# Kernel optimization log

Hardware: AMD Instinct MI355X
Metric: run time of the kernel (lower is better)

The kernel has to match this reference:

```python
import jax, jax.numpy as jnp
import numpy as np

B, T, C = 4, 2048, 1024
N_HEAD = 16
HEAD_DIM = C // N_HEAD


def setup_inputs() -> dict:
    key = jax.random.key(0)
    kx, kk, kq, kv, kp = jax.random.split(key, 5)
    s = 1.0 / np.sqrt(C)
    return {
        "x": jax.random.normal(kx, (B, T, C), dtype=jnp.float32),
        "Wk": jax.random.normal(kk, (C, C), dtype=jnp.float32) * s,
        "Wq": jax.random.normal(kq, (C, C), dtype=jnp.float32) * s,
        "Wv": jax.random.normal(kv, (C, C), dtype=jnp.float32) * s,
        "Wp": jax.random.normal(kp, (C, C), dtype=jnp.float32) * s,
    }


def reference(x, Wk, Wq, Wv, Wp):
    b, t, c = x.shape
    # torch nn.Linear(y = x @ W.T); split heads -> [B, H, T, D]
    def heads(w):
        return jnp.einsum("btc,ec->bte", x, w).reshape(b, t, N_HEAD, HEAD_DIM).transpose(0, 2, 1, 3)
    k = heads(Wk)
    q = heads(Wq)
    v = heads(Wv)
    scale = 1.0 / np.sqrt(HEAD_DIM).astype(np.float32)
    att = jnp.einsum("bhqd,bhkd->bhqk", q, k) * scale  # [B,H,T,T]
    causal = jnp.tril(jnp.ones((t, t), dtype=bool))
    att = jnp.where(causal[None, None], att, -jnp.inf)
    att = jax.nn.softmax(att, axis=-1)
    y = jnp.einsum("bhqk,bhkd->bhqd", att, v)  # [B,H,T,D]
    y = y.transpose(0, 2, 1, 3).reshape(b, t, c)
    return jnp.einsum("btc,ec->bte", y, Wp)
```

## Files before the change

### kernel.cpp

```cpp
#include <hip/hip_runtime.h>

typedef __bf16 bf16x8 __attribute__((ext_vector_type(8)));
typedef float f32x4 __attribute__((ext_vector_type(4)));
typedef float f32x16 __attribute__((ext_vector_type(16)));
typedef unsigned short u16x8 __attribute__((ext_vector_type(8)));
typedef unsigned short u16x4 __attribute__((ext_vector_type(4)));
typedef unsigned u32x4 __attribute__((ext_vector_type(4)));

#define BB 4
#define TT 2048
#define CC 1024
#define HH 16
#define DD 64

__device__ __forceinline__ unsigned short f2bf(float f){
  unsigned u = __builtin_bit_cast(unsigned, f);
  u += 0x7FFFu + ((u >> 16) & 1u);
  return (unsigned short)(u >> 16);
}
__device__ __forceinline__ bf16x8 as_bf(u16x8 v){ return __builtin_bit_cast(bf16x8, v); }
__device__ __forceinline__ unsigned cvt_pk(float lo, float hi){
  unsigned r; asm("v_cvt_pk_bf16_f32 %0, %1, %2" : "=v"(r) : "v"(lo), "v"(hi)); return r;
}
__device__ __forceinline__ void pl32swap(unsigned &a, unsigned &b){
  asm("v_permlane32_swap_b32 %0, %1" : "+v"(a), "+v"(b));
}
__device__ __forceinline__ float ex2(float x){
#if __has_builtin(__builtin_amdgcn_exp2f)
  return __builtin_amdgcn_exp2f(x);
#else
  return __expf(x * 0.6931471805599453f);
#endif
}

__global__ __launch_bounds__(256) void cvt_all(const float* __restrict__ x,
                                               const float* __restrict__ Wk,
                                               const float* __restrict__ Wq,
                                               const float* __restrict__ Wv,
                                               const float* __restrict__ Wp,
                                               unsigned short* __restrict__ xb,
                                               unsigned short* __restrict__ wb){
  const int i = blockIdx.x * 256 + threadIdx.x;
  constexpr int EX = (BB*TT*CC)/4;
  const float* src; unsigned short* dst; int off;
  if (i < EX){ src = x; dst = xb; off = i; }
  else {
    const int j = i - EX;
    const int wsel = j >> 18;
    off = j & 262143;
    src = (wsel==0) ? Wk : (wsel==1) ? Wq : (wsel==2) ? Wv : Wp;
    dst = wb + ((size_t)wsel << 20);
  }
  const float4 f = ((const float4*)src)[off];
  u16x4 o; o.x = f2bf(f.x); o.y = f2bf(f.y); o.z = f2bf(f.z); o.w = f2bf(f.w);
  ((u16x4*)dst)[off] = o;
}

template<int NX, bool QKV>
__global__ __launch_bounds__(256) void gemm128(const unsigned short* __restrict__ A,
                                               const unsigned short* __restrict__ Bm,
                                               void* __restrict__ o0, void* __restrict__ o1,
                                               void* __restrict__ o2){
  constexpr int K = 1024;
  constexpr int NWG = NX * 64;
  __shared__ __align__(16) unsigned short As[128*64];
  __shared__ __align__(16) unsigned short Bs[128*64];
  const int tid = threadIdx.x;
  const int flat = blockIdx.y * NX + blockIdx.x;
  const int swz = (flat & 7) * (NWG / 8) + (flat >> 3);
  const int n0 = (swz % NX) * 128;
  const int m0 = (swz / NX) * 128;
  const int w = tid >> 6, lane = tid & 63, l15 = lane & 15, g = lane >> 4;
  const int wm = (w >> 1) * 64, wn = (w & 1) * 64;

  f32x4 acc[4][4] = {};

  for (int k0 = 0; k0 < K; k0 += 64){
    #pragma unroll
    for (int i = 0; i < 4; ++i){
      const int p = i*256 + tid;
      const int r = p >> 3, c = p & 7;
      const int gc = c ^ (r & 7);
      __builtin_amdgcn_global_load_lds(
        (const __attribute__((address_space(1))) void*)(A + (size_t)(m0 + r)*K + k0 + gc*8),
        (__attribute__((address_space(3))) void*)(As + p*8), 16, 0, 0);
    }
    #pragma unroll
    for (int i = 0; i < 4; ++i){
      const int p = i*256 + tid;
      const int r = p >> 3, c = p & 7;
      const int gc = c ^ (r & 7);
      __builtin_amdgcn_global_load_lds(
        (const __attribute__((address_space(1))) void*)(Bm + (size_t)(n0 + r)*K + k0 + gc*8),
        (__attribute__((address_space(3))) void*)(Bs + p*8), 16, 0, 0);
    }
    __syncthreads();

    bf16x8 af[2][4], bfr[2][4];
    #pragma unroll
    for (int ks = 0; ks < 2; ++ks){
      #pragma unroll
      for (int m = 0; m < 4; ++m){
        const int R = wm + m*16 + l15;
        const int c = (ks*4 + g) ^ (R & 7);
        af[ks][m] = as_bf(*(const u16x8*)(As + R*64 + c*8));
      }
      #pragma unroll
      for (int n = 0; n < 4; ++n){
        const int R = wn + n*16 + l15;
        const int c = (ks*4 + g) ^ (R & 7);
        bfr[ks][n] = as_bf(*(const u16x8*)(Bs + R*64 + c*8));
      }
    }
    #pragma unroll
    for (int ks = 0; ks < 2; ++ks)
      #pragma unroll
      for (int m = 0; m < 4; ++m)
        #pragma unroll
        for (int n = 0; n < 4; ++n)
          acc[m][n] = __builtin_amdgcn_mfma_f32_16x16x32_bf16(af[ks][m], bfr[ks][n], acc[m][n], 0, 0, 0);
    __syncthreads();
  }

  const int tsel = n0 >> 10;
  const float sc = (QKV && tsel == 1) ? 0.18033688011112042f : 1.0f;
  unsigned short* outb = nullptr;
  if (QKV) outb = (unsigned short*)(tsel == 0 ? o0 : tsel == 1 ? o1 : o2);

  #pragma unroll
  for (int m = 0; m < 4; ++m)
    #pragma unroll
    for (int n = 0; n < 4; ++n)
      #pragma unroll
      for (int r = 0; r < 4; ++r){
        const int row = m0 + wm + m*16 + g*4 + r;
        const int col = n0 + wn + n*16 + l15;
        const float v = acc[m][n][r];
        if (QKV) outb[(size_t)row*1024 + (col & 1023)] = f2bf(v * sc);
        else     ((float*)o0)[(size_t)row*1024 + col] = v;
      }
}

__global__ __launch_bounds__(256) void transpose_v(const unsigned short* __restrict__ V,
                                                   unsigned short* __restrict__ Vt){
  __shared__ unsigned short Ts[64*72];
  const int kt = blockIdx.x, bh = blockIdx.y;
  const int b = bh >> 4, h = bh & 15;
  const int tid = threadIdx.x;
  #pragma unroll
  for (int i = 0; i < 2; ++i){
    const int p = i*256 + tid, r = p >> 3, c = p & 7;
    *(u16x8*)(Ts + r*72 + c*8) =
      *(const u16x8*)(V + (size_t)b*TT*CC + (size_t)(kt*64 + r)*CC + h*DD + c*8);
  }
  __syncthreads();
  #pragma unroll
  for (int i = 0; i < 2; ++i){
    const int p = i*256 + tid, d = p >> 3, c = p & 7;
    u16x8 v;
    #pragma unroll
    for (int j = 0; j < 8; ++j) v[j] = Ts[(c*8 + j)*72 + d];
    *(u16x8*)(Vt + ((size_t)bh*DD + d)*TT + (size_t)kt*64 + ((c ^ (d & 7))*8)) = v;
  }
}

__global__ __launch_bounds__(512, 4) void attn2(const unsigned short* __restrict__ Q,
                                                const unsigned short* __restrict__ Km,
                                                const unsigned short* __restrict__ Vt,
                                                unsigned short* __restrict__ Y){
  __shared__ __align__(16) unsigned short Ks[3][64*64];
  __shared__ __align__(16) unsigned short Vs[3][64*64];
  const int bh = blockIdx.x, b = bh >> 4, h = bh & 15;
  const int qt = 7 - blockIdx.y;
  const int tid = threadIdx.x;
  const int w = tid >> 6, lane = tid & 63, l31 = lane & 31, hi = lane >> 5;
  const int q0 = qt * 256;
  const int wq0 = q0 + w * 32;
  const int wqmax = wq0 + 31;
  const int nkt = 4 * qt + 4;
  const int qg = wq0 + l31;

  const unsigned short* Ksrc = Km + (size_t)b*TT*CC + h*DD;
  const unsigned short* Vsrc = Vt + (size_t)bh*DD*TT;

  auto stage = [&](int buf, int kt){
    const int r = tid >> 3, c = tid & 7;
    const int gc = c ^ (r & 7);
    __builtin_amdgcn_global_load_lds(
      (const __attribute__((address_space(1))) void*)(Ksrc + (size_t)(kt*64 + r)*CC + gc*8),
      (__attribute__((address_space(3))) void*)(&Ks[buf][tid*8]), 16, 0, 0);
    __builtin_amdgcn_global_load_lds(
      (const __attribute__((address_space(1))) void*)(Vsrc + (size_t)r*TT + (size_t)kt*64 + c*8),
      (__attribute__((address_space(3))) void*)(&Vs[buf][tid*8]), 16, 0, 0);
  };

  stage(0, 0);

  const unsigned short* qrow = Q + ((size_t)b*TT + wq0 + l31)*CC + h*DD;
  bf16x8 qf[4];
  #pragma unroll
  for (int ds = 0; ds < 4; ++ds)
    qf[ds] = as_bf(*(const u16x8*)(qrow + 16*ds + 8*hi));

  int koff[4];
  #pragma unroll
  for (int ds = 0; ds < 4; ++ds)
    koff[ds] = l31*64 + (((2*ds + hi) ^ (l31 & 7)) * 8);

  float m_ = -1e30f, l_ = 0.f;
  f32x16 y0 = {}, y1 = {};

  int cb = 0;
  for (int t = 0; t < nkt; ++t){
    const int nx = (cb == 2) ? 0 : cb + 1;
    if (t + 1 < nkt){
      stage(nx, t + 1);
      asm volatile("s_waitcnt vmcnt(2)" ::: "memory");
    } else {
      asm volatile("s_waitcnt vmcnt(0)" ::: "memory");
    }
    __builtin_amdgcn_s_barrier();

    if (t*64 <= wqmax){
      const unsigned short* Kp = &Ks[cb][0];
      const unsigned short* Vp = &Vs[cb][0];

      f32x16 s0 = {}, s1 = {};
      __builtin_amdgcn_s_setprio(1);
      #pragma unroll
      for (int ds = 0; ds < 4; ++ds){
        bf16x8 kf0 = as_bf(*(const u16x8*)(Kp + koff[ds]));
        s0 = __builtin_amdgcn_mfma_f32_32x32x16_bf16(kf0, qf[ds], s0, 0, 0, 0);
        bf16x8 kf1 = as_bf(*(const u16x8*)(Kp + koff[ds] + 2048));
        s1 = __builtin_amdgcn_mfma_f32_32x32x16_bf16(kf1, qf[ds], s1, 0, 0, 0);
      }
      __builtin_amdgcn_s_setprio(0);

      if (t*64 + 63 > wq0){
        const int kb0 = t*64;
        #pragma unroll
        for (int r = 0; r < 16; ++r){
          const int kr = (r & 3) + 8*(r >> 2) + 4*hi;
          if (kb0 + kr      > qg) s0[r] = -1e30f;
          if (kb0 + 32 + kr > qg) s1[r] = -1e30f;
        }
      }

      float tm[8];
      #pragma unroll
      for (int r = 0; r < 8; ++r) tm[r] = fmaxf(fmaxf(s0[r], s0[r+8]), fmaxf(s1[r], s1[r+8]));
      #pragma unroll
      for (int r = 0; r < 4; ++r) tm[r] = fmaxf(tm[r], tm[r+4]);
      float pmax = fmaxf(fmaxf(tm[0], tm[2]), fmaxf(tm[1], tm[3]));
      pmax = fmaxf(pmax, __shfl_xor(pmax, 32));

      if (!__all(pmax <= m_ + 8.f)){
        const float mnew = fmaxf(m_, pmax);
        const float alpha = ex2(m_ - mnew);
        l_ *= alpha;
        #pragma unroll
        for (int r = 0; r < 16; ++r){
          const float ar = __shfl(alpha, (r & 3) + 8*(r >> 2) + 4*hi);
          y0[r] *= ar; y1[r] *= ar;
        }
        m_ = mnew;
      }

      #pragma unroll
      for (int r = 0; r < 16; ++r) s0[r] = ex2(s0[r] - m_);
      #pragma unroll
      for (int r = 0; r < 16; ++r) s1[r] = ex2(s1[r] - m_);
      float ts[8];
      #pragma unroll
      for (int r = 0; r < 8; ++r) ts[r] = (s0[r] + s0[r+8]) + (s1[r] + s1[r+8]);
      #pragma unroll
      for (int r = 0; r < 4; ++r) ts[r] += ts[r+4];
      float rs = (ts[0] + ts[2]) + (ts[1] + ts[3]);
      rs += __shfl_xor(rs, 32);
      l_ += rs;

      __builtin_amdgcn_s_setprio(1);
      #pragma unroll
      for (int m = 0; m < 4; ++m){
        const f32x16 c = (m < 2) ? s0 : s1;
        const int bx = (m & 1) * 8;
        unsigned A0 = cvt_pk(c[bx+0], c[bx+1]);
        unsigned B0 = cvt_pk(c[bx+4], c[bx+5]);
        pl32swap(A0, B0);
        unsigned A1 = cvt_pk(c[bx+2], c[bx+3]);
        unsigned B1 = cvt_pk(c[bx+6], c[bx+7]);
        pl32swap(A1, B1);
        u32x4 pw; pw.x = A0; pw.y = A1; pw.z = B0; pw.w = B1;
        const bf16x8 pa = __builtin_bit_cast(bf16x8, pw);
        bf16x8 vf0 = as_bf(*(const u16x8*)(Vp + koff[m]));
        y0 = __builtin_amdgcn_mfma_f32_32x32x16_bf16(pa, vf0, y0, 0, 0, 0);
        bf16x8 vf1 = as_bf(*(const u16x8*)(Vp + koff[m] + 2048));
        y1 = __builtin_amdgcn_mfma_f32_32x32x16_bf16(pa, vf1, y1, 0, 0, 0);
      }
      __builtin_amdgcn_s_setprio(0);
    }
    cb = nx;
  }

  const float linv = 1.f / l_;
  #pragma unroll
  for (int r = 0; r < 16; ++r){
    const int qlr = (r & 3) + 8*(r >> 2) + 4*hi;
    const float lr = __shfl(linv, qlr);
    unsigned short* yp = Y + ((size_t)b*TT + wq0 + qlr)*CC + h*DD + l31;
    yp[0]  = f2bf(y0[r] * lr);
    yp[32] = f2bf(y1[r] * lr);
  }
}

extern "C" void kernel_launch(void* const* d_in, const int* in_sizes, int n_in,
                              void* d_out, int out_size, void* d_ws, size_t ws_size,
                              hipStream_t stream){
  const float* x  = (const float*)d_in[0];
  const float* Wk = (const float*)d_in[1];
  const float* Wq = (const float*)d_in[2];
  const float* Wv = (const float*)d_in[3];
  const float* Wp = (const float*)d_in[4];

  const size_t E  = (size_t)BB*TT*CC;
  const size_t Wn = (size_t)CC*CC;
  unsigned short* ws  = (unsigned short*)d_ws;
  unsigned short* xb  = ws;
  unsigned short* wkb = xb  + E;
  unsigned short* wqb = wkb + Wn;
  unsigned short* wvb = wqb + Wn;
  unsigned short* wpb = wvb + Wn;
  unsigned short* qb  = wpb + Wn;
  unsigned short* kb  = qb  + E;
  unsigned short* vb  = kb  + E;
  unsigned short* vt  = vb  + E;

  cvt_all<<<12288, 256, 0, stream>>>(x, Wk, Wq, Wv, Wp, xb, wkb);

  gemm128<24, true><<<dim3(24, 64), 256, 0, stream>>>(xb, wkb, kb, qb, vb);

  transpose_v<<<dim3(TT/64, BB*HH), 256, 0, stream>>>(vb, vt);

  unsigned short* yb = xb;
  attn2<<<dim3(BB*HH, TT/256), 512, 0, stream>>>(qb, kb, vt, yb);

  gemm128<8, false><<<dim3(8, 64), 256, 0, stream>>>(yb, wpb, (float*)d_out, nullptr, nullptr);
}
```

Measured before the change: 164.2 us.

## Give each attention wave two query tiles and deepen K/V prefetch

The attention kernel now runs 256 threads per block, and each wave handles 64 query rows as two 32-row tiles. Each K/V fragment read from LDS therefore feeds two MFMAs, halving LDS reads per unit of math. The K/V staging ring grows from 3 to 4 buffers with a prefetch distance of two tiles to hide global load latency. This raises register pressure (four score and four output accumulators per wave), and with fewer waves per block, causal-skip imbalance across waves could leave some waves idle longer.

```diff
diff --git a/kernel.cpp b/kernel.cpp
--- a/kernel.cpp
+++ b/kernel.cpp
@@ -164,153 +164,179 @@
   }
 }
 
-__global__ __launch_bounds__(512, 4) void attn2(const unsigned short* __restrict__ Q,
+__global__ __launch_bounds__(256, 2) void attn3(const unsigned short* __restrict__ Q,
                                                 const unsigned short* __restrict__ Km,
                                                 const unsigned short* __restrict__ Vt,
                                                 unsigned short* __restrict__ Y){
-  __shared__ __align__(16) unsigned short Ks[3][64*64];
-  __shared__ __align__(16) unsigned short Vs[3][64*64];
-  const int bh = blockIdx.x, b = bh >> 4, h = bh & 15;
+  __shared__ __align__(16) unsigned short Ks[4][64*64];
+  __shared__ __align__(16) unsigned short Vs[4][64*64];
+  const int bh = blockIdx.x, b = bh >> 4, hd = bh & 15;
   const int qt = 7 - blockIdx.y;
   const int tid = threadIdx.x;
   const int w = tid >> 6, lane = tid & 63, l31 = lane & 31, hi = lane >> 5;
-  const int q0 = qt * 256;
-  const int wq0 = q0 + w * 32;
-  const int wqmax = wq0 + 31;
-  const int nkt = 4 * qt + 4;
-  const int qg = wq0 + l31;
-
-  const unsigned short* Ksrc = Km + (size_t)b*TT*CC + h*DD;
+  const int nkt = 4*qt + 4;
+  const int qbase = qt*256 + w*64;
+  const int tD = 4*qt + w;
+  const int qga = qbase + l31, qgb = qbase + 32 + l31;
+
+  const unsigned short* Ksrc = Km + (size_t)b*TT*CC + hd*DD;
   const unsigned short* Vsrc = Vt + (size_t)bh*DD*TT;
 
   auto stage = [&](int buf, int kt){
-    const int r = tid >> 3, c = tid & 7;
-    const int gc = c ^ (r & 7);
-    __builtin_amdgcn_global_load_lds(
-      (const __attribute__((address_space(1))) void*)(Ksrc + (size_t)(kt*64 + r)*CC + gc*8),
-      (__attribute__((address_space(3))) void*)(&Ks[buf][tid*8]), 16, 0, 0);
-    __builtin_amdgcn_global_load_lds(
-      (const __attribute__((address_space(1))) void*)(Vsrc + (size_t)r*TT + (size_t)kt*64 + c*8),
-      (__attribute__((address_space(3))) void*)(&Vs[buf][tid*8]), 16, 0, 0);
+    #pragma unroll
+    for (int i = 0; i < 2; ++i){
+      const int rr = (tid >> 3) + i*32, c = tid & 7;
+      const int gc = c ^ (rr & 7);
+      __builtin_amdgcn_global_load_lds(
+        (const __attribute__((address_space(1))) void*)(Ksrc + (size_t)(kt*64 + rr)*CC + gc*8),
+        (__attribute__((address_space(3))) void*)(&Ks[buf][(i*256 + tid)*8]), 16, 0, 0);
+      __builtin_amdgcn_global_load_lds(
+        (const __attribute__((address_space(1))) void*)(Vsrc + (size_t)rr*TT + (size_t)kt*64 + c*8),
+        (__attribute__((address_space(3))) void*)(&Vs[buf][(i*256 + tid)*8]), 16, 0, 0);
+    }
   };
 
   stage(0, 0);
-
-  const unsigned short* qrow = Q + ((size_t)b*TT + wq0 + l31)*CC + h*DD;
-  bf16x8 qf[4];
-  #pragma unroll
-  for (int ds = 0; ds < 4; ++ds)
-    qf[ds] = as_bf(*(const u16x8*)(qrow + 16*ds + 8*hi));
+  stage(1, 1);
+
+  const unsigned short* qra = Q + ((size_t)b*TT + qbase + l31)*CC + hd*DD;
+  bf16x8 qfA[4], qfB[4];
+  #pragma unroll
+  for (int ds = 0; ds < 4; ++ds){
+    qfA[ds] = as_bf(*(const u16x8*)(qra + 16*ds + 8*hi));
+    qfB[ds] = as_bf(*(const u16x8*)(qra + 32*CC + 16*ds + 8*hi));
+  }
 
   int koff[4];
   #pragma unroll
   for (int ds = 0; ds < 4; ++ds)
     koff[ds] = l31*64 + (((2*ds + hi) ^ (l31 & 7)) * 8);
 
-  float m_ = -1e30f, l_ = 0.f;
-  f32x16 y0 = {}, y1 = {};
-
-  int cb = 0;
+  float mA = -1e30f, lA = 0.f, mB = -1e30f, lB = 0.f;
+  f32x16 yA0 = {}, yA1 = {}, yB0 = {}, yB1 = {};
+
+  auto sm = [&](f32x16& s0, f32x16& s1, float& m_, float& l_, f32x16& y0, f32x16& y1){
+    float tm[8];
+    #pragma unroll
+    for (int r = 0; r < 8; ++r) tm[r] = fmaxf(fmaxf(s0[r], s0[r+8]), fmaxf(s1[r], s1[r+8]));
+    #pragma unroll
+    for (int r = 0; r < 4; ++r) tm[r] = fmaxf(tm[r], tm[r+4]);
+    float pmax = fmaxf(fmaxf(tm[0], tm[2]), fmaxf(tm[1], tm[3]));
+    pmax = fmaxf(pmax, __shfl_xor(pmax, 32));
+    if (!__all(pmax <= m_ + 8.f)){
+      const float mnew = fmaxf(m_, pmax);
+      const float alpha = ex2(m_ - mnew);
+      l_ *= alpha;
+      #pragma unroll
+      for (int r = 0; r < 16; ++r){
+        const float ar = __shfl(alpha, (r & 3) + 8*(r >> 2) + 4*hi);
+        y0[r] *= ar; y1[r] *= ar;
+      }
+      m_ = mnew;
+    }
+    #pragma unroll
+    for (int r = 0; r < 16; ++r) s0[r] = ex2(s0[r] - m_);
+    #pragma unroll
+    for (int r = 0; r < 16; ++r) s1[r] = ex2(s1[r] - m_);
+    float ts[8];
+    #pragma unroll
+    for (int r = 0; r < 8; ++r) ts[r] = (s0[r] + s0[r+8]) + (s1[r] + s1[r+8]);
+    #pragma unroll
+    for (int r = 0; r < 4; ++r) ts[r] += ts[r+4];
+    float rs = (ts[0] + ts[2]) + (ts[1] + ts[3]);
+    rs += __shfl_xor(rs, 32);
+    l_ += rs;
+  };
+
+  auto pack = [&](const f32x16& s0, const f32x16& s1, bf16x8* pa){
+    #pragma unroll
+    for (int m = 0; m < 4; ++m){
+      const f32x16& c = (m < 2) ? s0 : s1;
+      const int bx = (m & 1) * 8;
+      unsigned A0 = cvt_pk(c[bx+0], c[bx+1]);
+      unsigned B0 = cvt_pk(c[bx+4], c[bx+5]);
+      pl32swap(A0, B0);
+      unsigned A1 = cvt_pk(c[bx+2], c[bx+3]);
+      unsigned B1 = cvt_pk(c[bx+6], c[bx+7]);
+      pl32swap(A1, B1);
+      u32x4 pw; pw.x = A0; pw.y = A1; pw.z = B0; pw.w = B1;
+      pa[m] = __builtin_bit_cast(bf16x8, pw);
+    }
+  };
+
   for (int t = 0; t < nkt; ++t){
-    const int nx = (cb == 2) ? 0 : cb + 1;
-    if (t + 1 < nkt){
-      stage(nx, t + 1);
-      asm volatile("s_waitcnt vmcnt(2)" ::: "memory");
+    if (t + 2 < nkt){
+      stage((t + 2) & 3, t + 2);
+      asm volatile("s_waitcnt vmcnt(8)" ::: "memory");
+    } else if (t + 1 < nkt){
+      asm volatile("s_waitcnt vmcnt(4)" ::: "memory");
     } else {
       asm volatile("s_waitcnt vmcnt(0)" ::: "memory");
     }
     __builtin_amdgcn_s_barrier();
-
-    if (t*64 <= wqmax){
-      const unsigned short* Kp = &Ks[cb][0];
-      const unsigned short* Vp = &Vs[cb][0];
-
-      f32x16 s0 = {}, s1 = {};
-      __builtin_amdgcn_s_setprio(1);
-      #pragma unroll
-      for (int ds = 0; ds < 4; ++ds){
-        bf16x8 kf0 = as_bf(*(const u16x8*)(Kp + koff[ds]));
-        s0 = __builtin_amdgcn_mfma_f32_32x32x16_bf16(kf0, qf[ds], s0, 0, 0, 0);
-        bf16x8 kf1 = as_bf(*(const u16x8*)(Kp + koff[ds] + 2048));
-        s1 = __builtin_amdgcn_mfma_f32_32x32x16_bf16(kf1, qf[ds], s1, 0, 0, 0);
-      }
-      __builtin_amdgcn_s_setprio(0);
-
-      if (t*64 + 63 > wq0){
-        const int kb0 = t*64;
-        #pragma unroll
-        for (int r = 0; r < 16; ++r){
-          const int kr = (r & 3) + 8*(r >> 2) + 4*hi;
-          if (kb0 + kr      > qg) s0[r] = -1e30f;
-          if (kb0 + 32 + kr > qg) s1[r] = -1e30f;
-        }
-      }
-
-      float tm[8];
-      #pragma unroll
-      for (int r = 0; r < 8; ++r) tm[r] = fmaxf(fmaxf(s0[r], s0[r+8]), fmaxf(s1[r], s1[r+8]));
-      #pragma unroll
-      for (int r = 0; r < 4; ++r) tm[r] = fmaxf(tm[r], tm[r+4]);
-      float pmax = fmaxf(fmaxf(tm[0], tm[2]), fmaxf(tm[1], tm[3]));
-      pmax = fmaxf(pmax, __shfl_xor(pmax, 32));
-
-      if (!__all(pmax <= m_ + 8.f)){
-        const float mnew = fmaxf(m_, pmax);
-        const float alpha = ex2(m_ - mnew);
-        l_ *= alpha;
-        #pragma unroll
-        for (int r = 0; r < 16; ++r){
-          const float ar = __shfl(alpha, (r & 3) + 8*(r >> 2) + 4*hi);
-          y0[r] *= ar; y1[r] *= ar;
-        }
-        m_ = mnew;
-      }
-
-      #pragma unroll
-      for (int r = 0; r < 16; ++r) s0[r] = ex2(s0[r] - m_);
-      #pragma unroll
-      for (int r = 0; r < 16; ++r) s1[r] = ex2(s1[r] - m_);
-      float ts[8];
-      #pragma unroll
-      for (int r = 0; r < 8; ++r) ts[r] = (s0[r] + s0[r+8]) + (s1[r] + s1[r+8]);
-      #pragma unroll
-      for (int r = 0; r < 4; ++r) ts[r] += ts[r+4];
-      float rs = (ts[0] + ts[2]) + (ts[1] + ts[3]);
-      rs += __shfl_xor(rs, 32);
-      l_ += rs;
-
-      __builtin_amdgcn_s_setprio(1);
-      #pragma unroll
-      for (int m = 0; m < 4; ++m){
-        const f32x16 c = (m < 2) ? s0 : s1;
-        const int bx = (m & 1) * 8;
-        unsigned A0 = cvt_pk(c[bx+0], c[bx+1]);
-        unsigned B0 = cvt_pk(c[bx+4], c[bx+5]);
-        pl32swap(A0, B0);
-        unsigned A1 = cvt_pk(c[bx+2], c[bx+3]);
-        unsigned B1 = cvt_pk(c[bx+6], c[bx+7]);
-        pl32swap(A1, B1);
-        u32x4 pw; pw.x = A0; pw.y = A1; pw.z = B0; pw.w = B1;
-        const bf16x8 pa = __builtin_bit_cast(bf16x8, pw);
-        bf16x8 vf0 = as_bf(*(const u16x8*)(Vp + koff[m]));
-        y0 = __builtin_amdgcn_mfma_f32_32x32x16_bf16(pa, vf0, y0, 0, 0, 0);
-        bf16x8 vf1 = as_bf(*(const u16x8*)(Vp + koff[m] + 2048));
-        y1 = __builtin_amdgcn_mfma_f32_32x32x16_bf16(pa, vf1, y1, 0, 0, 0);
-      }
-      __builtin_amdgcn_s_setprio(0);
-    }
-    cb = nx;
-  }
-
-  const float linv = 1.f / l_;
-  #pragma unroll
-  for (int r = 0; r < 16; ++r){
-    const int qlr = (r & 3) + 8*(r >> 2) + 4*hi;
-    const float lr = __shfl(linv, qlr);
-    unsigned short* yp = Y + ((size_t)b*TT + wq0 + qlr)*CC + h*DD + l31;
-    yp[0]  = f2bf(y0[r] * lr);
-    yp[32] = f2bf(y1[r] * lr);
-  }
+    if (t > tD) continue;
+
+    const unsigned short* Kp = &Ks[t & 3][0];
+    const unsigned short* Vp = &Vs[t & 3][0];
+
+    f32x16 sA0 = {}, sA1 = {}, sB0 = {}, sB1 = {};
+    __builtin_amdgcn_s_setprio(1);
+    #pragma unroll
+    for (int ds = 0; ds < 4; ++ds){
+      bf16x8 kf0 = as_bf(*(const u16x8*)(Kp + koff[ds]));
+      sA0 = __builtin_amdgcn_mfma_f32_32x32x16_bf16(kf0, qfA[ds], sA0, 0, 0, 0);
+      sB0 = __builtin_amdgcn_mfma_f32_32x32x16_bf16(kf0, qfB[ds], sB0, 0, 0, 0);
+      bf16x8 kf1 = as_bf(*(const u16x8*)(Kp + koff[ds] + 2048));
+      sA1 = __builtin_amdgcn_mfma_f32_32x32x16_bf16(kf1, qfA[ds], sA1, 0, 0, 0);
+      sB1 = __builtin_amdgcn_mfma_f32_32x32x16_bf16(kf1, qfB[ds], sB1, 0, 0, 0);
+    }
+    __builtin_amdgcn_s_setprio(0);
+
+    if (t == tD){
+      const int kb0 = t*64;
+      #pragma unroll
+      for (int r = 0; r < 16; ++r){
+        const int kr = (r & 3) + 8*(r >> 2) + 4*hi;
+        if (kb0 + kr      > qga) sA0[r] = -1e30f;
+        if (kb0 + 32 + kr > qga) sA1[r] = -1e30f;
+        if (kb0 + kr      > qgb) sB0[r] = -1e30f;
+        if (kb0 + 32 + kr > qgb) sB1[r] = -1e30f;
+      }
+    }
+
+    sm(sA0, sA1, mA, lA, yA0, yA1);
+    sm(sB0, sB1, mB, lB, yB0, yB1);
+
+    bf16x8 paA[4], paB[4];
+    pack(sA0, sA1, paA);
+    pack(sB0, sB1, paB);
+
+    __builtin_amdgcn_s_setprio(1);
+    #pragma unroll
+    for (int m = 0; m < 4; ++m){
+      bf16x8 vf0 = as_bf(*(const u16x8*)(Vp + koff[m]));
+      yA0 = __builtin_amdgcn_mfma_f32_32x32x16_bf16(paA[m], vf0, yA0, 0, 0, 0);
+      yB0 = __builtin_amdgcn_mfma_f32_32x32x16_bf16(paB[m], vf0, yB0, 0, 0, 0);
+      bf16x8 vf1 = as_bf(*(const u16x8*)(Vp + koff[m] + 2048));
+      yA1 = __builtin_amdgcn_mfma_f32_32x32x16_bf16(paA[m], vf1, yA1, 0, 0, 0);
+      yB1 = __builtin_amdgcn_mfma_f32_32x32x16_bf16(paB[m], vf1, yB1, 0, 0, 0);
+    }
+    __builtin_amdgcn_s_setprio(0);
+  }
+
+  auto wr = [&](const f32x16& y0, const f32x16& y1, float l_, int qb){
+    const float linv = 1.f / l_;
+    #pragma unroll
+    for (int r = 0; r < 16; ++r){
+      const int qlr = (r & 3) + 8*(r >> 2) + 4*hi;
+      const float lr = __shfl(linv, qlr);
+      unsigned short* yp = Y + ((size_t)b*TT + qb + qlr)*CC + hd*DD + l31;
+      yp[0]  = f2bf(y0[r] * lr);
+      yp[32] = f2bf(y1[r] * lr);
+    }
+  };
+  wr(yA0, yA1, lA, qbase);
+  wr(yB0, yB1, lB, qbase + 32);
 }
 
 extern "C" void kernel_launch(void* const* d_in, const int* in_sizes, int n_in,
@@ -342,7 +368,7 @@
   transpose_v<<<dim3(TT/64, BB*HH), 256, 0, stream>>>(vb, vt);
 
   unsigned short* yb = xb;
-  attn2<<<dim3(BB*HH, TT/256), 512, 0, stream>>>(qb, kb, vt, yb);
+  attn3<<<dim3(BB*HH, TT/256), 256, 0, stream>>>(qb, kb, vt, yb);
 
   gemm128<8, false><<<dim3(8, 64), 256, 0, stream>>>(yb, wpb, (float*)d_out, nullptr, nullptr);
 }
```

Result: slower. 177.2 us (+7.9%).

## Double-buffer GEMM LDS tiles and reorder attention query-tile scheduling

Applied to the files above, without the earlier changes.

The 128x128 GEMM kernel now keeps two LDS buffers for its A and B tiles. It issues the async global-to-LDS loads for the next K tile before computing the current one, using explicit vmcnt waits and raw barriers, so load latency can overlap with MFMA work. Separately, the attention kernel maps blockIdx.y to query tiles as 7,6,5,4 and then 0,1,2,3 instead of strictly descending, which changes how heavy and light causal blocks are dispatched. Doubling the shared memory per GEMM block may lower occupancy. The raw s_barrier has no implicit LDS fence, so correctness depends on the hand-written waitcnt.

```diff
diff --git a/kernel.cpp b/kernel.cpp
--- a/kernel.cpp
+++ b/kernel.cpp
@@ -62,9 +62,10 @@
                                                void* __restrict__ o0, void* __restrict__ o1,
                                                void* __restrict__ o2){
   constexpr int K = 1024;
+  constexpr int NKT = K / 64;
   constexpr int NWG = NX * 64;
-  __shared__ __align__(16) unsigned short As[128*64];
-  __shared__ __align__(16) unsigned short Bs[128*64];
+  __shared__ __align__(16) unsigned short As[2][128*64];
+  __shared__ __align__(16) unsigned short Bs[2][128*64];
   const int tid = threadIdx.x;
   const int flat = blockIdx.y * NX + blockIdx.x;
   const int swz = (flat & 7) * (NWG / 8) + (flat >> 3);
@@ -73,9 +74,7 @@
   const int w = tid >> 6, lane = tid & 63, l15 = lane & 15, g = lane >> 4;
   const int wm = (w >> 1) * 64, wn = (w & 1) * 64;
 
-  f32x4 acc[4][4] = {};
-
-  for (int k0 = 0; k0 < K; k0 += 64){
+  auto stage = [&](int d, int k0){
     #pragma unroll
     for (int i = 0; i < 4; ++i){
       const int p = i*256 + tid;
@@ -83,7 +82,7 @@
       const int gc = c ^ (r & 7);
       __builtin_amdgcn_global_load_lds(
         (const __attribute__((address_space(1))) void*)(A + (size_t)(m0 + r)*K + k0 + gc*8),
-        (__attribute__((address_space(3))) void*)(As + p*8), 16, 0, 0);
+        (__attribute__((address_space(3))) void*)(&As[d][p*8]), 16, 0, 0);
     }
     #pragma unroll
     for (int i = 0; i < 4; ++i){
@@ -92,9 +91,22 @@
       const int gc = c ^ (r & 7);
       __builtin_amdgcn_global_load_lds(
         (const __attribute__((address_space(1))) void*)(Bm + (size_t)(n0 + r)*K + k0 + gc*8),
-        (__attribute__((address_space(3))) void*)(Bs + p*8), 16, 0, 0);
-    }
-    __syncthreads();
+        (__attribute__((address_space(3))) void*)(&Bs[d][p*8]), 16, 0, 0);
+    }
+  };
+
+  f32x4 acc[4][4] = {};
+  stage(0, 0);
+
+  for (int kt = 0; kt < NKT; ++kt){
+    const int d = kt & 1;
+    if (kt + 1 < NKT){
+      stage(d ^ 1, (kt + 1) * 64);
+      asm volatile("s_waitcnt vmcnt(8)" ::: "memory");
+    } else {
+      asm volatile("s_waitcnt vmcnt(0)" ::: "memory");
+    }
+    __builtin_amdgcn_s_barrier();
 
     bf16x8 af[2][4], bfr[2][4];
     #pragma unroll
@@ -103,13 +115,13 @@
       for (int m = 0; m < 4; ++m){
         const int R = wm + m*16 + l15;
         const int c = (ks*4 + g) ^ (R & 7);
-        af[ks][m] = as_bf(*(const u16x8*)(As + R*64 + c*8));
+        af[ks][m] = as_bf(*(const u16x8*)(&As[d][R*64 + c*8]));
       }
       #pragma unroll
       for (int n = 0; n < 4; ++n){
         const int R = wn + n*16 + l15;
         const int c = (ks*4 + g) ^ (R & 7);
-        bfr[ks][n] = as_bf(*(const u16x8*)(Bs + R*64 + c*8));
+        bfr[ks][n] = as_bf(*(const u16x8*)(&Bs[d][R*64 + c*8]));
       }
     }
     #pragma unroll
@@ -119,7 +131,8 @@
         #pragma unroll
         for (int n = 0; n < 4; ++n)
           acc[m][n] = __builtin_amdgcn_mfma_f32_16x16x32_bf16(af[ks][m], bfr[ks][n], acc[m][n], 0, 0, 0);
-    __syncthreads();
+
+    __builtin_amdgcn_s_barrier();
   }
 
   const int tsel = n0 >> 10;
@@ -171,7 +184,8 @@
   __shared__ __align__(16) unsigned short Ks[3][64*64];
   __shared__ __align__(16) unsigned short Vs[3][64*64];
   const int bh = blockIdx.x, b = bh >> 4, h = bh & 15;
-  const int qt = 7 - blockIdx.y;
+  const int yq = blockIdx.y;
+  const int qt = (yq < 4) ? (7 - yq) : (yq - 4);
   const int tid = threadIdx.x;
   const int w = tid >> 6, lane = tid & 63, l31 = lane & 31, hi = lane >> 5;
   const int q0 = qt * 256;
```

New measurement: 163.5 us. Within noise of the previous version (-0.4%).

## Stage 128-key tiles with double buffering and reorder query-tile scheduling

Applied to the files above, without the earlier changes.

The attention kernel now loads two 64-key K/V subtiles per stage into a 2-deep buffer instead of single 64-key tiles into a 3-deep ring, which halves the number of barriers and waitcnts per key range. It also maps blockIdx.y so the first four blocks take the heaviest query tiles and the rest take the lightest, changing how the causal workload is spread. The cost is a full vmcnt(0) wait at the end of each iteration, so loads now overlap with only one stage of compute. LDS use rises from 48KB to 64KB, which may reduce occupancy at the declared 4 blocks per CU.

```diff
diff --git a/kernel.cpp b/kernel.cpp
--- a/kernel.cpp
+++ b/kernel.cpp
@@ -168,30 +168,35 @@
                                                 const unsigned short* __restrict__ Km,
                                                 const unsigned short* __restrict__ Vt,
                                                 unsigned short* __restrict__ Y){
-  __shared__ __align__(16) unsigned short Ks[3][64*64];
-  __shared__ __align__(16) unsigned short Vs[3][64*64];
+  __shared__ __align__(16) unsigned short Ks[2][8192];
+  __shared__ __align__(16) unsigned short Vs[2][8192];
   const int bh = blockIdx.x, b = bh >> 4, h = bh & 15;
-  const int qt = 7 - blockIdx.y;
+  const int yq = blockIdx.y;
+  const int qt = (yq < 4) ? (7 - yq) : (yq - 4);
   const int tid = threadIdx.x;
   const int w = tid >> 6, lane = tid & 63, l31 = lane & 31, hi = lane >> 5;
   const int q0 = qt * 256;
   const int wq0 = q0 + w * 32;
   const int wqmax = wq0 + 31;
-  const int nkt = 4 * qt + 4;
+  const int nt = 2 * qt + 2;
   const int qg = wq0 + l31;
 
   const unsigned short* Ksrc = Km + (size_t)b*TT*CC + h*DD;
   const unsigned short* Vsrc = Vt + (size_t)bh*DD*TT;
 
-  auto stage = [&](int buf, int kt){
+  auto stage = [&](int buf, int t){
     const int r = tid >> 3, c = tid & 7;
     const int gc = c ^ (r & 7);
-    __builtin_amdgcn_global_load_lds(
-      (const __attribute__((address_space(1))) void*)(Ksrc + (size_t)(kt*64 + r)*CC + gc*8),
-      (__attribute__((address_space(3))) void*)(&Ks[buf][tid*8]), 16, 0, 0);
-    __builtin_amdgcn_global_load_lds(
-      (const __attribute__((address_space(1))) void*)(Vsrc + (size_t)r*TT + (size_t)kt*64 + c*8),
-      (__attribute__((address_space(3))) void*)(&Vs[buf][tid*8]), 16, 0, 0);
+    #pragma unroll
+    for (int s = 0; s < 2; ++s){
+      const int kt64 = 2*t + s;
+      __builtin_amdgcn_global_load_lds(
+        (const __attribute__((address_space(1))) void*)(Ksrc + (size_t)(kt64*64 + r)*CC + gc*8),
+        (__attribute__((address_space(3))) void*)(&Ks[buf][s*4096 + tid*8]), 16, 0, 0);
+      __builtin_amdgcn_global_load_lds(
+        (const __attribute__((address_space(1))) void*)(Vsrc + (size_t)r*TT + (size_t)kt64*64 + c*8),
+        (__attribute__((address_space(3))) void*)(&Vs[buf][s*4096 + tid*8]), 16, 0, 0);
+    }
   };
 
   stage(0, 0);
@@ -210,20 +215,19 @@
   float m_ = -1e30f, l_ = 0.f;
   f32x16 y0 = {}, y1 = {};
 
-  int cb = 0;
-  for (int t = 0; t < nkt; ++t){
-    const int nx = (cb == 2) ? 0 : cb + 1;
-    if (t + 1 < nkt){
-      stage(nx, t + 1);
-      asm volatile("s_waitcnt vmcnt(2)" ::: "memory");
-    } else {
-      asm volatile("s_waitcnt vmcnt(0)" ::: "memory");
-    }
-    __builtin_amdgcn_s_barrier();
-
-    if (t*64 <= wqmax){
-      const unsigned short* Kp = &Ks[cb][0];
-      const unsigned short* Vp = &Vs[cb][0];
+  asm volatile("s_waitcnt vmcnt(0)" ::: "memory");
+  __builtin_amdgcn_s_barrier();
+
+  for (int t = 0; t < nt; ++t){
+    const int cur = t & 1;
+    if (t + 1 < nt) stage(cur ^ 1, t + 1);
+
+    #pragma unroll
+    for (int s = 0; s < 2; ++s){
+      const int kb0 = t*128 + s*64;
+      if (kb0 > wqmax) continue;
+      const unsigned short* Kp = &Ks[cur][s*4096];
+      const unsigned short* Vp = &Vs[cur][s*4096];
 
       f32x16 s0 = {}, s1 = {};
       __builtin_amdgcn_s_setprio(1);
@@ -236,8 +240,7 @@
       }
       __builtin_amdgcn_s_setprio(0);
 
-      if (t*64 + 63 > wq0){
-        const int kb0 = t*64;
+      if (kb0 + 63 > wq0){
         #pragma unroll
         for (int r = 0; r < 16; ++r){
           const int kr = (r & 3) + 8*(r >> 2) + 4*hi;
@@ -299,7 +302,11 @@
       }
       __builtin_amdgcn_s_setprio(0);
     }
-    cb = nx;
+
+    if (t + 1 < nt){
+      asm volatile("s_waitcnt vmcnt(0)" ::: "memory");
+      __builtin_amdgcn_s_barrier();
+    }
   }
 
   const float linv = 1.f / l_;
```

Measured after the change: 163.0 us. Within noise of the previous version (-0.7%).
